# Kernel tuning notes

Measured on AMD Instinct MI355X. Metric: run time of the kernel, lower is better.

Reference implementation:

```python
import jax, jax.numpy as jnp
import numpy as np

N_QUBITS = 20
SUPPORT = (3, 8, 15)   # qubit_support
BATCH = 8
DIM = 2 ** len(SUPPORT)  # 8


def setup_inputs() -> dict:
    key = jax.random.key(0)
    ks = jax.random.split(key, 5)
    state_shape = (2,) * N_QUBITS + (BATCH,)
    state_real = jax.random.normal(ks[0], state_shape, dtype=jnp.float32)
    state_imag = jax.random.normal(ks[1], state_shape, dtype=jnp.float32)
    a = jax.random.normal(ks[2], (DIM, DIM), dtype=jnp.float32)
    b = jax.random.normal(ks[3], (DIM, DIM), dtype=jnp.float32)
    h_real = ((a + a.T) * 0.5)[..., None]   # (DIM, DIM, 1) symmetric
    h_imag = ((b - b.T) * 0.5)[..., None]   # antisymmetric -> H Hermitian
    t = jax.random.uniform(ks[4], (BATCH,), dtype=jnp.float32)
    return {"state_real": state_real, "state_imag": state_imag,
            "h_real": h_real, "h_imag": h_imag, "t": t}


def reference(state_real, state_imag, h_real, h_imag, t):
    # state: (2,)*N_QUBITS + (BATCH,) complex
    state = state_real + 1j * state_imag
    # Hermitian generator, hmat layout (d, d, batch_h=1) as in the module buffer
    H = (h_real + 1j * h_imag)[..., 0]                      # (DIM, DIM)
    # _unitary: expm(-1j * t * H) per batch. H Hermitian -> exact via eigh.
    w, V = jnp.linalg.eigh(H)                               # w real (DIM,), V (DIM, DIM)
    phases = jnp.exp(-1j * (t[:, None] * w[None, :]))       # (BATCH, DIM)
    U = jnp.einsum('ik,bk,jk->bij', V, phases, V.conj())    # (BATCH, DIM, DIM)
    # apply_operator: reshape U into per-qubit indices and contract at SUPPORT axes
    s = len(SUPPORT)
    op = U.reshape((BATCH,) + (2,) * (2 * s))               # (B, out bits..., in bits...)
    B_LBL = 100
    out_lbls = [200 + i for i in range(s)]
    op_axes = [B_LBL] + out_lbls + list(SUPPORT)
    state_axes = list(range(N_QUBITS)) + [B_LBL]
    out_axes = list(range(N_QUBITS))
    for i, q in enumerate(SUPPORT):
        out_axes[q] = out_lbls[i]
    out_axes = out_axes + [B_LBL]
    return jnp.einsum(op, op_axes, state, state_axes, out_axes)
```

## Files before the change

### kernel.cpp

```cpp
#include <hip/hip_runtime.h>


#define SUP_OFF(m) ( ((m)&4 ? 524288u : 0u) + ((m)&2 ? 16384u : 0u) + ((m)&1 ? 128u : 0u) )

__global__ void expm_kernel(const float* __restrict__ h_real,
                            const float* __restrict__ h_imag,
                            const float* __restrict__ t_g,
                            float2* __restrict__ U2)
{
    __shared__ float Tre[8][64], Tim[8][64];
    __shared__ float Mre[8][64], Mim[8][64];
    __shared__ float Ere[8][64], Eim[8][64];

    const int tid = threadIdx.x;
    const int b   = tid >> 5;
    const int e0  = tid & 31;
    const int e1  = e0 + 32;
    const int o0 = e0 >> 3, i0 = e0 & 7;
    const int o1 = e1 >> 3, i1 = e1 & 7;

    const float sc   = t_g[b] * (1.0f / 32.0f);
    const float m0re =  sc * h_imag[e0];
    const float m0im = -sc * h_real[e0];
    const float m1re =  sc * h_imag[e1];
    const float m1im = -sc * h_real[e1];

    Mre[b][e0] = m0re; Mim[b][e0] = m0im;
    Mre[b][e1] = m1re; Mim[b][e1] = m1im;
    Tre[b][e0] = m0re; Tim[b][e0] = m0im;
    Tre[b][e1] = m1re; Tim[b][e1] = m1im;
    float a0re = (o0 == i0 ? 1.f : 0.f) + m0re, a0im = m0im;
    float a1re = (o1 == i1 ? 1.f : 0.f) + m1re, a1im = m1im;
    __syncthreads();

    for (int k = 2; k <= 10; ++k) {
        float s0re = 0.f, s0im = 0.f, s1re = 0.f, s1im = 0.f;
        #pragma unroll
        for (int j = 0; j < 8; ++j) {
            float tre = Tre[b][o0 * 8 + j], tim = Tim[b][o0 * 8 + j];
            float mre = Mre[b][j * 8 + i0], mim = Mim[b][j * 8 + i0];
            s0re += tre * mre - tim * mim;
            s0im += tre * mim + tim * mre;
            tre = Tre[b][o1 * 8 + j]; tim = Tim[b][o1 * 8 + j];
            mre = Mre[b][j * 8 + i1]; mim = Mim[b][j * 8 + i1];
            s1re += tre * mre - tim * mim;
            s1im += tre * mim + tim * mre;
        }
        const float inv = 1.0f / (float)k;
        s0re *= inv; s0im *= inv; s1re *= inv; s1im *= inv;
        __syncthreads();
        Tre[b][e0] = s0re; Tim[b][e0] = s0im;
        Tre[b][e1] = s1re; Tim[b][e1] = s1im;
        a0re += s0re; a0im += s0im;
        a1re += s1re; a1im += s1im;
        __syncthreads();
    }

    Ere[b][e0] = a0re; Eim[b][e0] = a0im;
    Ere[b][e1] = a1re; Eim[b][e1] = a1im;
    __syncthreads();

    for (int sq = 0; sq < 5; ++sq) {
        float s0re = 0.f, s0im = 0.f, s1re = 0.f, s1im = 0.f;
        #pragma unroll
        for (int j = 0; j < 8; ++j) {
            float xre = Ere[b][o0 * 8 + j], xim = Eim[b][o0 * 8 + j];
            float yre = Ere[b][j * 8 + i0], yim = Eim[b][j * 8 + i0];
            s0re += xre * yre - xim * yim;
            s0im += xre * yim + xim * yre;
            xre = Ere[b][o1 * 8 + j]; xim = Eim[b][o1 * 8 + j];
            yre = Ere[b][j * 8 + i1]; yim = Eim[b][j * 8 + i1];
            s1re += xre * yre - xim * yim;
            s1im += xre * yim + xim * yre;
        }
        __syncthreads();
        if (sq < 4) {
            Ere[b][e0] = s0re; Eim[b][e0] = s0im;
            Ere[b][e1] = s1re; Eim[b][e1] = s1im;
            __syncthreads();
        } else {
            U2[b * 64 + e0] = make_float2(s0re, s0im);
            U2[b * 64 + e1] = make_float2(s1re, s1im);
        }
    }
}

__global__ __launch_bounds__(256) void apply_kernel(
        const float* __restrict__ sre_g,
        const float* __restrict__ sim_g,
        const float2* __restrict__ U2,
        float* __restrict__ out)
{
    __shared__ alignas(16) float2 uLds[8 * 66];
    const int tid = threadIdx.x;
    for (int v = tid; v < 512; v += 256) {
        uLds[(v >> 6) * 66 + (v & 63)] = U2[v];
    }
    __syncthreads();

    const int bid = ((blockIdx.x & 7) << 9) | (blockIdx.x >> 3);

    const int r = bid * 256 + tid;
    const int b = r & 7;

    const unsigned addr = (r & 0x7Fu)
                        | ((r & 0x1F80u)  << 1)
                        | ((r & 0x1E000u) << 2)
                        | ((r & 0xE0000u) << 3);

    float xre[8], xim[8];
    #pragma unroll
    for (int i = 0; i < 8; ++i) {
        const unsigned off = addr + SUP_OFF(i);
        xre[i] = sre_g[off];
        xim[i] = sim_g[off];
    }

    const float4* urow = reinterpret_cast<const float4*>(uLds) + b * 33;

    #pragma unroll
    for (int o = 0; o < 8; ++o) {
        float are = 0.f;
        #pragma unroll
        for (int p = 0; p < 4; ++p) {
            const float4 u = urow[o * 4 + p];
            const int i0 = 2 * p, i1 = 2 * p + 1;
            are += u.x * xre[i0] - u.y * xim[i0];
            are += u.z * xre[i1] - u.w * xim[i1];
        }
        __builtin_nontemporal_store(are, out + addr + SUP_OFF(o));
    }
}

extern "C" void kernel_launch(void* const* d_in, const int* in_sizes, int n_in,
                              void* d_out, int out_size, void* d_ws, size_t ws_size,
                              hipStream_t stream) {
    const float* state_real = (const float*)d_in[0];
    const float* state_imag = (const float*)d_in[1];
    const float* h_real     = (const float*)d_in[2];
    const float* h_imag     = (const float*)d_in[3];
    const float* t          = (const float*)d_in[4];

    float2* U2 = (float2*)d_ws;

    expm_kernel<<<1, 256, 0, stream>>>(h_real, h_imag, t, U2);

    apply_kernel<<<4096, 256, 0, stream>>>(state_real, state_imag, U2,
                                           (float*)d_out);
}
```

Measured before the change: 29.57 us.

## Process two batch entries per thread with float2 loads and repacked U layout

The apply kernel now gives each thread a pair of adjacent batch elements. State loads and output stores become float2 accesses, and the grid is halved to 2048 blocks. The expm kernel writes U in a new float4 layout that interleaves the two batches, giving each thread conflict-free LDS reads. The block-index swizzle and the nontemporal stores are dropped, and launch bounds now request 8 blocks per SM. The goal is fewer, wider memory instructions. In exchange each thread holds more registers and there are fewer waves to hide latency.

```diff
diff --git a/kernel.cpp b/kernel.cpp
--- a/kernel.cpp
+++ b/kernel.cpp
@@ -6,7 +6,7 @@
 __global__ void expm_kernel(const float* __restrict__ h_real,
                             const float* __restrict__ h_imag,
                             const float* __restrict__ t_g,
-                            float2* __restrict__ U2)
+                            float4* __restrict__ U4)
 {
     __shared__ float Tre[8][64], Tim[8][64];
     __shared__ float Mre[8][64], Mim[8][64];
@@ -38,13 +38,13 @@
         #pragma unroll
         for (int j = 0; j < 8; ++j) {
             float tre = Tre[b][o0 * 8 + j], tim = Tim[b][o0 * 8 + j];
-            float mre = Mre[b][j * 8 + i0], mim = Mim[b][j * 8 + i0];
-            s0re += tre * mre - tim * mim;
-            s0im += tre * mim + tim * mre;
+            float qre = Mre[b][j * 8 + i0], qim = Mim[b][j * 8 + i0];
+            s0re += tre * qre - tim * qim;
+            s0im += tre * qim + tim * qre;
             tre = Tre[b][o1 * 8 + j]; tim = Tim[b][o1 * 8 + j];
-            mre = Mre[b][j * 8 + i1]; mim = Mim[b][j * 8 + i1];
-            s1re += tre * mre - tim * mim;
-            s1im += tre * mim + tim * mre;
+            qre = Mre[b][j * 8 + i1]; qim = Mim[b][j * 8 + i1];
+            s1re += tre * qre - tim * qim;
+            s1im += tre * qim + tim * qre;
         }
         const float inv = 1.0f / (float)k;
         s0re *= inv; s0im *= inv; s1re *= inv; s1im *= inv;
@@ -74,61 +74,79 @@
             s1im += xre * yim + xim * yre;
         }
         __syncthreads();
-        if (sq < 4) {
-            Ere[b][e0] = s0re; Eim[b][e0] = s0im;
-            Ere[b][e1] = s1re; Eim[b][e1] = s1im;
-            __syncthreads();
-        } else {
-            U2[b * 64 + e0] = make_float2(s0re, s0im);
-            U2[b * 64 + e1] = make_float2(s1re, s1im);
-        }
+        Ere[b][e0] = s0re; Eim[b][e0] = s0im;
+        Ere[b][e1] = s1re; Eim[b][e1] = s1im;
+        __syncthreads();
+    }
+
+    {
+        const int o  = tid & 7;
+        const int bp = (tid >> 3) & 3;
+        const int i  = tid >> 5;
+        const int e  = o * 8 + i;
+        const int b0 = 2 * bp, b1 = 2 * bp + 1;
+        U4[tid] = make_float4(Ere[b0][e], Eim[b0][e], Ere[b1][e], Eim[b1][e]);
     }
 }
 
-__global__ __launch_bounds__(256) void apply_kernel(
+__global__ __launch_bounds__(256, 8) void apply_kernel(
         const float* __restrict__ sre_g,
         const float* __restrict__ sim_g,
-        const float2* __restrict__ U2,
+        const float4* __restrict__ U4,
         float* __restrict__ out)
 {
-    __shared__ alignas(16) float2 uLds[8 * 66];
+    __shared__ alignas(16) float4 uL[8 * 4 * 9];
     const int tid = threadIdx.x;
-    for (int v = tid; v < 512; v += 256) {
-        uLds[(v >> 6) * 66 + (v & 63)] = U2[v];
+    {
+        const int ib = tid >> 3, o = tid & 7;
+        uL[ib * 9 + o] = U4[tid];
     }
     __syncthreads();
 
-    const int bid = ((blockIdx.x & 7) << 9) | (blockIdx.x >> 3);
+    const unsigned t   = blockIdx.x * 256u + tid;
+    const unsigned rho = t >> 2;
+    const int      bp  = t & 3;
 
-    const int r = bid * 256 + tid;
-    const int b = r & 7;
+    const unsigned oct = (rho & 0xFu)
+                       | ((rho & 0x3F0u)   << 1)
+                       | ((rho & 0x3C00u)  << 2)
+                       | ((rho & 0x1C000u) << 3);
+    const unsigned base = (oct << 3) + 2u * bp;
 
-    const unsigned addr = (r & 0x7Fu)
-                        | ((r & 0x1F80u)  << 1)
-                        | ((r & 0x1E000u) << 2)
-                        | ((r & 0xE0000u) << 3);
+    float2 acc[8];
+    #pragma unroll
+    for (int o = 0; o < 8; ++o) acc[o] = make_float2(0.f, 0.f);
 
-    float xre[8], xim[8];
     #pragma unroll
-    for (int i = 0; i < 8; ++i) {
-        const unsigned off = addr + SUP_OFF(i);
-        xre[i] = sre_g[off];
-        xim[i] = sim_g[off];
+    for (int ip = 0; ip < 4; ++ip) {
+        const int ia = 2 * ip, ib2 = 2 * ip + 1;
+        const unsigned offa = base + SUP_OFF(ia);
+        const unsigned offb = base + SUP_OFF(ib2);
+
+        const float2 xra = *(const float2*)(sre_g + offa);
+        const float2 xia = *(const float2*)(sim_g + offa);
+        const float2 xrb = *(const float2*)(sre_g + offb);
+        const float2 xib = *(const float2*)(sim_g + offb);
+
+        const float4* uqa = &uL[(ia  * 4 + bp) * 9];
+        const float4* uqb = &uL[(ib2 * 4 + bp) * 9];
+        #pragma unroll
+        for (int o = 0; o < 8; ++o) {
+            const float4 qa = uqa[o];
+            acc[o].x += qa.x * xra.x - qa.y * xia.x;
+            acc[o].y += qa.z * xra.y - qa.w * xia.y;
+        }
+        #pragma unroll
+        for (int o = 0; o < 8; ++o) {
+            const float4 qb = uqb[o];
+            acc[o].x += qb.x * xrb.x - qb.y * xib.x;
+            acc[o].y += qb.z * xrb.y - qb.w * xib.y;
+        }
     }
-
-    const float4* urow = reinterpret_cast<const float4*>(uLds) + b * 33;
 
     #pragma unroll
     for (int o = 0; o < 8; ++o) {
-        float are = 0.f;
-        #pragma unroll
-        for (int p = 0; p < 4; ++p) {
-            const float4 u = urow[o * 4 + p];
-            const int i0 = 2 * p, i1 = 2 * p + 1;
-            are += u.x * xre[i0] - u.y * xim[i0];
-            are += u.z * xre[i1] - u.w * xim[i1];
-        }
-        __builtin_nontemporal_store(are, out + addr + SUP_OFF(o));
+        *(float2*)(out + base + SUP_OFF(o)) = acc[o];
     }
 }
 
@@ -141,10 +159,10 @@
     const float* h_imag     = (const float*)d_in[3];
     const float* t          = (const float*)d_in[4];
 
-    float2* U2 = (float2*)d_ws;
+    float4* U4 = (float4*)d_ws;
 
-    expm_kernel<<<1, 256, 0, stream>>>(h_real, h_imag, t, U2);
+    expm_kernel<<<1, 256, 0, stream>>>(h_real, h_imag, t, U4);
 
-    apply_kernel<<<4096, 256, 0, stream>>>(state_real, state_imag, U2,
+    apply_kernel<<<2048, 256, 0, stream>>>(state_real, state_imag, U4,
                                            (float*)d_out);
 }
```

After: 34.29 us. 1.16x slower.
